# Kernel optimization log

Measured on AMD Instinct MI355X. Metric: run time of the kernel, lower is better.

## Reference

```python
import jax, jax.numpy as jnp
import numpy as np


def setup_inputs() -> dict:
    key = jax.random.key(0)
    k1, k2, k3, k4, k5 = jax.random.split(key, 5)
    return {
        "d1": jax.random.normal(k1, (2, 4096, 512), dtype=jnp.float32),
        "d2": jax.random.normal(k2, (2, 512, 4096), dtype=jnp.float32),
        "d3": jax.random.normal(k3, (2, 4096, 512), dtype=jnp.float32),
        "d4": jax.random.normal(k4, (512, 512), dtype=jnp.float32),
        "d5": jax.random.normal(k5, (1, 512), dtype=jnp.float32),
    }


def reference(d1, d2, d3, d4, d5):
    # attention core: scores = d1 @ d2 -> [2, 4096, 4096]
    scores = jnp.einsum('bsd,bdt->bst', d1, d2)
    attn = jax.nn.softmax(scores, axis=2)
    # weighted values: [2, 4096, 512]
    ctx = jnp.einsum('bst,btd->bsd', attn, d3)
    # flatten batch*seq and apply final projection with bias (addmm)
    x = ctx.reshape(8192, 512)
    return d5 + x @ d4  # d5 [1,512] broadcasts over rows
```

## Files before the change

kernel.cpp:

```cpp
#include <hip/hip_runtime.h>

typedef unsigned short u16;
typedef __attribute__((ext_vector_type(8))) short short8;
typedef __attribute__((ext_vector_type(4))) float f32x4;

#define MFMA16(a, b, c) __builtin_amdgcn_mfma_f32_16x16x32_bf16((a), (b), (c), 0, 0, 0)

constexpr int Bb = 2, Ss = 4096, Tt = 4096, Dd = 512;
constexpr int BM = 64, BN = 64, TP = 4;
constexpr int TPART = Tt / TP;
constexpr int TCH = TPART / BN;

constexpr size_t SZ_BF = (size_t)Bb * Ss * Dd * 2;
constexpr size_t O_QH  = 0;
constexpr size_t O_QL  = O_QH + SZ_BF;
constexpr size_t O_D2TH = O_QL + SZ_BF;
constexpr size_t O_D2TL = O_D2TH + SZ_BF;
constexpr size_t O_D3T  = O_D2TL + SZ_BF;
constexpr size_t O_D4T  = O_D3T + SZ_BF;
constexpr size_t O_CTX  = O_D4T + (size_t)512 * 512 * 2;
constexpr size_t O_OP   = O_CTX + SZ_BF;
constexpr size_t O_MP   = O_OP + (size_t)TP * SZ_BF;
constexpr size_t O_LP   = O_MP + (size_t)TP * Bb * Ss * 4;

__device__ __forceinline__ u16 f2bf(float x) {
  union { float f; unsigned u; } v; v.f = x;
  unsigned r = v.u + 0x7fffu + ((v.u >> 16) & 1u);
  return (u16)(r >> 16);
}
__device__ __forceinline__ float bf2f(u16 h) {
  union { unsigned u; float f; } v; v.u = ((unsigned)h) << 16;
  return v.f;
}

__global__ void cvt_split_kernel(const float* __restrict__ in,
                                 u16* __restrict__ outh, u16* __restrict__ outl) {
  const int i = blockIdx.x * 256 + threadIdx.x;
  float4 v = ((const float4*)in)[i];
  ushort4 hh, ll;
  hh.x = f2bf(v.x); ll.x = f2bf(v.x - bf2f(hh.x));
  hh.y = f2bf(v.y); ll.y = f2bf(v.y - bf2f(hh.y));
  hh.z = f2bf(v.z); ll.z = f2bf(v.z - bf2f(hh.z));
  hh.w = f2bf(v.w); ll.w = f2bf(v.w - bf2f(hh.w));
  ((ushort4*)outh)[i] = hh;
  ((ushort4*)outl)[i] = ll;
}

__global__ void transpose_split_kernel(const float* __restrict__ in,
                                       u16* __restrict__ outh,
                                       u16* __restrict__ outl,
                                       int R, int C) {
  __shared__ float tile[32][33];
  int b = blockIdx.z;
  const float* inb = in + (size_t)b * R * C;
  int x = blockIdx.x * 32 + threadIdx.x;
  int y0 = blockIdx.y * 32;
  for (int j = threadIdx.y; j < 32; j += 8)
    tile[j][threadIdx.x] = inb[(size_t)(y0 + j) * C + x];
  __syncthreads();
  size_t ob = (size_t)b * C * R;
  for (int j = threadIdx.y; j < 32; j += 8) {
    float v = tile[threadIdx.x][j];
    size_t oi = ob + (size_t)(blockIdx.x * 32 + j) * R + (y0 + threadIdx.x);
    u16 h = f2bf(v);
    outh[oi] = h;
    if (outl) outl[oi] = f2bf(v - bf2f(h));
  }
}

__global__ __launch_bounds__(256, 2)
void flash_part_kernel(const u16* __restrict__ qh_g,
                       const u16* __restrict__ ql_g,
                       const u16* __restrict__ d2th,
                       const u16* __restrict__ d2tl,
                       const u16* __restrict__ d3t,
                       u16* __restrict__ opart,
                       float* __restrict__ mpart,
                       float* __restrict__ lpart) {
  __shared__ u16 kh[64 * 136], kl[64 * 136];
  __shared__ u16 vb[128 * 72];
  __shared__ u16 ph[64 * 72];

  const int tid = threadIdx.x;
  const int wave = tid >> 6, lane = tid & 63, quad = lane >> 4, l15 = lane & 15;
  const int m0 = wave * 16;
  const int s0 = blockIdx.x * BM, tp = blockIdx.y, b = blockIdx.z;

  f32x4 o_acc[32];
#pragma unroll
  for (int i = 0; i < 32; i++) o_acc[i] = (f32x4){0.f, 0.f, 0.f, 0.f};
  float m_r[4] = {-INFINITY, -INFINITY, -INFINITY, -INFINITY};
  float l_r[4] = {0.f, 0.f, 0.f, 0.f};

  const u16* qh_row = qh_g + ((size_t)b * Ss + s0 + m0 + l15) * Dd + quad * 8;
  const u16* ql_row = ql_g + ((size_t)b * Ss + s0 + m0 + l15) * Dd + quad * 8;
  const u16* kh_b = d2th + (size_t)b * Tt * Dd;
  const u16* kl_b = d2tl + (size_t)b * Tt * Dd;
  const u16* v_b  = d3t  + (size_t)b * Dd * Tt;

  const int krow = tid >> 2, kcol = (tid & 3) * 32;
  const int vrow = tid >> 1, vcol = (tid & 1) * 32;

  for (int tc = 0; tc < TCH; tc++) {
    const int t0 = tp * TPART + tc * BN;
    f32x4 s_acc[4];
#pragma unroll
    for (int nt = 0; nt < 4; nt++) s_acc[nt] = (f32x4){0.f, 0.f, 0.f, 0.f};

    for (int ds = 0; ds < 4; ds++) {
      const int d0 = ds * 128;
      __syncthreads();
      {
        const u16* sh = kh_b + (size_t)(t0 + krow) * Dd + d0 + kcol;
        const u16* sl = kl_b + (size_t)(t0 + krow) * Dd + d0 + kcol;
        u16* dh = &kh[krow * 136 + kcol];
        u16* dl = &kl[krow * 136 + kcol];
#pragma unroll
        for (int u = 0; u < 32; u += 8) {
          *(uint4*)(dh + u) = *(const uint4*)(sh + u);
          *(uint4*)(dl + u) = *(const uint4*)(sl + u);
        }
      }
      __syncthreads();
      short8 ah[4], al[4];
#pragma unroll
      for (int ks = 0; ks < 4; ks++) {
        ah[ks] = *(const short8*)(qh_row + d0 + ks * 32);
        al[ks] = *(const short8*)(ql_row + d0 + ks * 32);
      }
#pragma unroll
      for (int ks = 0; ks < 4; ks++) {
        const int kk = ks * 32 + quad * 8;
#pragma unroll
        for (int nt = 0; nt < 4; nt++) {
          short8 bh = *(const short8*)&kh[(nt * 16 + l15) * 136 + kk];
          short8 bl = *(const short8*)&kl[(nt * 16 + l15) * 136 + kk];
          s_acc[nt] = MFMA16(ah[ks], bh, s_acc[nt]);
          s_acc[nt] = MFMA16(al[ks], bh, s_acc[nt]);
          s_acc[nt] = MFMA16(ah[ks], bl, s_acc[nt]);
        }
      }
    }

    float alpha[4], psum[4];
#pragma unroll
    for (int r = 0; r < 4; r++) {
      float v = fmaxf(fmaxf(s_acc[0][r], s_acc[1][r]), fmaxf(s_acc[2][r], s_acc[3][r]));
      v = fmaxf(v, __shfl_xor(v, 1));
      v = fmaxf(v, __shfl_xor(v, 2));
      v = fmaxf(v, __shfl_xor(v, 4));
      v = fmaxf(v, __shfl_xor(v, 8));
      float mn = fmaxf(m_r[r], v);
      alpha[r] = __expf(m_r[r] - mn);
      m_r[r] = mn;
      psum[r] = 0.f;
    }
#pragma unroll
    for (int nt = 0; nt < 4; nt++) {
#pragma unroll
      for (int r = 0; r < 4; r++) {
        float p = __expf(s_acc[nt][r] - m_r[r]);
        psum[r] += p;
        ph[(m0 + quad * 4 + r) * 72 + nt * 16 + l15] = f2bf(p);
      }
    }
#pragma unroll
    for (int r = 0; r < 4; r++) {
      float v = psum[r];
      v += __shfl_xor(v, 1);
      v += __shfl_xor(v, 2);
      v += __shfl_xor(v, 4);
      v += __shfl_xor(v, 8);
      l_r[r] = l_r[r] * alpha[r] + v;
    }
#pragma unroll
    for (int j = 0; j < 32; j++) {
#pragma unroll
      for (int r = 0; r < 4; r++) o_acc[j][r] *= alpha[r];
    }

#pragma unroll
    for (int nc = 0; nc < 4; nc++) {
      __syncthreads();
      {
        const u16* sv = v_b + (size_t)(nc * 128 + vrow) * Tt + t0 + vcol;
        u16* dv = &vb[vrow * 72 + vcol];
#pragma unroll
        for (int u = 0; u < 32; u += 8) *(uint4*)(dv + u) = *(const uint4*)(sv + u);
      }
      __syncthreads();
#pragma unroll
      for (int ks = 0; ks < 2; ks++) {
        const int kk = ks * 32 + quad * 8;
        short8 ap = *(const short8*)&ph[(m0 + l15) * 72 + kk];
#pragma unroll
        for (int nt = 0; nt < 8; nt++) {
          short8 bv = *(const short8*)&vb[(nt * 16 + l15) * 72 + kk];
          o_acc[nc * 8 + nt] = MFMA16(ap, bv, o_acc[nc * 8 + nt]);
        }
      }
    }
  }

  const size_t obase = (((size_t)tp * Bb + b) * Ss + s0) * Dd;
#pragma unroll
  for (int j = 0; j < 32; j++) {
    const int col = (j >> 3) * 128 + (j & 7) * 16 + l15;
#pragma unroll
    for (int r = 0; r < 4; r++) {
      const int row = m0 + quad * 4 + r;
      opart[obase + (size_t)row * Dd + col] = f2bf(o_acc[j][r]);
    }
  }
  if (l15 == 0) {
    const size_t sbase = ((size_t)tp * Bb + b) * Ss + s0;
#pragma unroll
    for (int r = 0; r < 4; r++) {
      const int row = m0 + quad * 4 + r;
      mpart[sbase + row] = m_r[r];
      lpart[sbase + row] = l_r[r];
    }
  }
}

__global__ void combine_kernel(const u16* __restrict__ opart,
                               const float* __restrict__ mpart,
                               const float* __restrict__ lpart,
                               u16* __restrict__ ctx) {
  const int idx = blockIdx.x * blockDim.x + threadIdx.x;
  const int vpr = Dd / 8;
  const int row = idx / vpr;
  const int dv = (idx % vpr) * 8;
  float mv[TP], mM = -INFINITY;
#pragma unroll
  for (int p = 0; p < TP; p++) {
    mv[p] = mpart[(size_t)p * Bb * Ss + row];
    mM = fmaxf(mM, mv[p]);
  }
  float w[TP], denom = 0.f;
#pragma unroll
  for (int p = 0; p < TP; p++) {
    float e = __expf(mv[p] - mM);
    w[p] = e;
    denom += e * lpart[(size_t)p * Bb * Ss + row];
  }
  const float inv = 1.0f / denom;
  float acc[8];
#pragma unroll
  for (int e = 0; e < 8; e++) acc[e] = 0.f;
#pragma unroll
  for (int p = 0; p < TP; p++) {
    uint4 raw = *(const uint4*)&opart[(size_t)p * Bb * Ss * Dd + (size_t)row * Dd + dv];
    const u16* u = (const u16*)&raw;
#pragma unroll
    for (int e = 0; e < 8; e++) acc[e] += w[p] * bf2f(u[e]);
  }
  u16 outv[8];
#pragma unroll
  for (int e = 0; e < 8; e++) outv[e] = f2bf(acc[e] * inv);
  *(uint4*)&ctx[(size_t)row * Dd + dv] = *(const uint4*)outv;
}

__global__ __launch_bounds__(256, 2)
void proj_kernel(const u16* __restrict__ ctx,
                 const u16* __restrict__ d4t,
                 const float* __restrict__ d5,
                 float* __restrict__ out) {
  __shared__ u16 a_lds[128 * 40], b_lds[128 * 40];
  const int tid = threadIdx.x;
  const int wave = tid >> 6, lane = tid & 63, quad = lane >> 4, l15 = lane & 15;
  const int m0w = (wave & 1) * 64, n0w = (wave >> 1) * 64;
  const int bm = blockIdx.x, bn = blockIdx.y;
  f32x4 acc[4][4];
#pragma unroll
  for (int i = 0; i < 4; i++)
#pragma unroll
    for (int j = 0; j < 4; j++) acc[i][j] = (f32x4){0.f, 0.f, 0.f, 0.f};

  const int srow = tid >> 2, scol = (tid & 3) * 8;
  for (int kt = 0; kt < 16; kt++) {
    const int k0 = kt * 32;
    __syncthreads();
#pragma unroll
    for (int pass = 0; pass < 2; pass++) {
      const int row = srow + pass * 64;
      *(uint4*)&a_lds[row * 40 + scol] =
          *(const uint4*)&ctx[(size_t)(bm * 128 + row) * Dd + k0 + scol];
      *(uint4*)&b_lds[row * 40 + scol] =
          *(const uint4*)&d4t[(size_t)(bn * 128 + row) * Dd + k0 + scol];
    }
    __syncthreads();
    short8 af[4], bfr[4];
#pragma unroll
    for (int i = 0; i < 4; i++)
      af[i] = *(const short8*)&a_lds[(m0w + 16 * i + l15) * 40 + quad * 8];
#pragma unroll
    for (int j = 0; j < 4; j++)
      bfr[j] = *(const short8*)&b_lds[(n0w + 16 * j + l15) * 40 + quad * 8];
#pragma unroll
    for (int i = 0; i < 4; i++)
#pragma unroll
      for (int j = 0; j < 4; j++) acc[i][j] = MFMA16(af[i], bfr[j], acc[i][j]);
  }
#pragma unroll
  for (int j = 0; j < 4; j++) {
    const int colg = bn * 128 + n0w + 16 * j + l15;
    const float bias = d5[colg];
#pragma unroll
    for (int i = 0; i < 4; i++) {
#pragma unroll
      for (int r = 0; r < 4; r++) {
        const int rowg = bm * 128 + m0w + 16 * i + quad * 4 + r;
        out[(size_t)rowg * 512 + colg] = acc[i][j][r] + bias;
      }
    }
  }
}

extern "C" void kernel_launch(void* const* d_in, const int* in_sizes, int n_in,
                              void* d_out, int out_size, void* d_ws, size_t ws_size,
                              hipStream_t stream) {
  (void)in_sizes; (void)n_in; (void)out_size; (void)ws_size;
  const float* d1 = (const float*)d_in[0];
  const float* d2 = (const float*)d_in[1];
  const float* d3 = (const float*)d_in[2];
  const float* d4 = (const float*)d_in[3];
  const float* d5 = (const float*)d_in[4];
  float* out = (float*)d_out;
  char* ws = (char*)d_ws;

  u16* qh_g = (u16*)(ws + O_QH);
  u16* ql_g = (u16*)(ws + O_QL);
  u16* d2th = (u16*)(ws + O_D2TH);
  u16* d2tl = (u16*)(ws + O_D2TL);
  u16* d3t  = (u16*)(ws + O_D3T);
  u16* d4t  = (u16*)(ws + O_D4T);
  u16* ctx  = (u16*)(ws + O_CTX);
  u16* opart = (u16*)(ws + O_OP);
  float* mpart = (float*)(ws + O_MP);
  float* lpart = (float*)(ws + O_LP);

  cvt_split_kernel<<<(Bb * Ss * Dd / 4) / 256, 256, 0, stream>>>(d1, qh_g, ql_g);
  transpose_split_kernel<<<dim3(128, 16, 2), dim3(32, 8), 0, stream>>>(d2, d2th, d2tl, 512, 4096);
  transpose_split_kernel<<<dim3(16, 128, 2), dim3(32, 8), 0, stream>>>(d3, d3t, nullptr, 4096, 512);
  transpose_split_kernel<<<dim3(16, 16, 1), dim3(32, 8), 0, stream>>>(d4, d4t, nullptr, 512, 512);

  flash_part_kernel<<<dim3(Ss / BM, TP, Bb), 256, 0, stream>>>(qh_g, ql_g, d2th, d2tl, d3t,
                                                               opart, mpart, lpart);
  combine_kernel<<<(Bb * Ss * Dd / 8) / 256, 256, 0, stream>>>(opart, mpart, lpart, ctx);
  proj_kernel<<<dim3(64, 4), 256, 0, stream>>>(ctx, d4t, d5, out);
}
```

Baseline: 516.9 us.

## Swizzle LDS tiles for K, V and P, and raise wave priority around MFMA

Writes the K-high/K-low, V and probability tiles into LDS with a rotating 8-element group swizzle on top of the existing padding, and applies the same index mapping on the MFMA operand reads. The goal is fewer LDS bank conflicts on the short8 fragment loads. The P fragments are now loaded once per key chunk rather than once per value chunk, and the Q register loads move ahead of the barrier. s_setprio brackets the MFMA loops so waves issuing matrix instructions get scheduling priority. This adds some integer index arithmetic per load.

Measured after the change: 560.9 us. 1.09x slower.

```diff
diff --git a/kernel.cpp b/kernel.cpp
--- a/kernel.cpp
+++ b/kernel.cpp
@@ -113,33 +113,38 @@
       {
         const u16* sh = kh_b + (size_t)(t0 + krow) * Dd + d0 + kcol;
         const u16* sl = kl_b + (size_t)(t0 + krow) * Dd + d0 + kcol;
-        u16* dh = &kh[krow * 136 + kcol];
-        u16* dl = &kl[krow * 136 + kcol];
-#pragma unroll
-        for (int u = 0; u < 32; u += 8) {
-          *(uint4*)(dh + u) = *(const uint4*)(sh + u);
-          *(uint4*)(dl + u) = *(const uint4*)(sl + u);
+        const int gb = kcol >> 3;
+#pragma unroll
+        for (int j = 0; j < 4; j++) {
+          const int g = gb + j;
+          const int s = ((g + 2 * krow) & 7) | (g & 8);
+          *(uint4*)&kh[krow * 136 + s * 8] = *(const uint4*)(sh + j * 8);
+          *(uint4*)&kl[krow * 136 + s * 8] = *(const uint4*)(sl + j * 8);
         }
       }
-      __syncthreads();
       short8 ah[4], al[4];
 #pragma unroll
       for (int ks = 0; ks < 4; ks++) {
         ah[ks] = *(const short8*)(qh_row + d0 + ks * 32);
         al[ks] = *(const short8*)(ql_row + d0 + ks * 32);
       }
+      __syncthreads();
+      __builtin_amdgcn_s_setprio(1);
 #pragma unroll
       for (int ks = 0; ks < 4; ks++) {
-        const int kk = ks * 32 + quad * 8;
+        const int g0 = ks * 4 + quad;
+        const int sg = ((g0 + 2 * l15) & 7) | (g0 & 8);
 #pragma unroll
         for (int nt = 0; nt < 4; nt++) {
-          short8 bh = *(const short8*)&kh[(nt * 16 + l15) * 136 + kk];
-          short8 bl = *(const short8*)&kl[(nt * 16 + l15) * 136 + kk];
+          const int off = (nt * 16 + l15) * 136 + sg * 8;
+          short8 bh = *(const short8*)&kh[off];
+          short8 bl = *(const short8*)&kl[off];
           s_acc[nt] = MFMA16(ah[ks], bh, s_acc[nt]);
           s_acc[nt] = MFMA16(al[ks], bh, s_acc[nt]);
           s_acc[nt] = MFMA16(ah[ks], bl, s_acc[nt]);
         }
       }
+      __builtin_amdgcn_s_setprio(0);
     }
 
     float alpha[4], psum[4];
@@ -161,7 +166,8 @@
       for (int r = 0; r < 4; r++) {
         float p = __expf(s_acc[nt][r] - m_r[r]);
         psum[r] += p;
-        ph[(m0 + quad * 4 + r) * 72 + nt * 16 + l15] = f2bf(p);
+        const int sp = (2 * nt + (l15 >> 3) + 2 * r) & 7;
+        ph[(m0 + quad * 4 + r) * 72 + sp * 8 + (l15 & 7)] = f2bf(p);
       }
     }
 #pragma unroll
@@ -179,26 +185,40 @@
       for (int r = 0; r < 4; r++) o_acc[j][r] *= alpha[r];
     }
 
+    short8 ap[2];
+#pragma unroll
+    for (int ks = 0; ks < 2; ks++) {
+      const int g0 = ks * 4 + quad;
+      const int sg = (g0 + 2 * l15) & 7;
+      ap[ks] = *(const short8*)&ph[(m0 + l15) * 72 + sg * 8];
+    }
+
 #pragma unroll
     for (int nc = 0; nc < 4; nc++) {
       __syncthreads();
       {
         const u16* sv = v_b + (size_t)(nc * 128 + vrow) * Tt + t0 + vcol;
-        u16* dv = &vb[vrow * 72 + vcol];
-#pragma unroll
-        for (int u = 0; u < 32; u += 8) *(uint4*)(dv + u) = *(const uint4*)(sv + u);
+        const int gb = vcol >> 3;
+#pragma unroll
+        for (int j = 0; j < 4; j++) {
+          const int g = gb + j;
+          const int s = (g + 2 * vrow) & 7;
+          *(uint4*)&vb[vrow * 72 + s * 8] = *(const uint4*)(sv + j * 8);
+        }
       }
       __syncthreads();
+      __builtin_amdgcn_s_setprio(1);
 #pragma unroll
       for (int ks = 0; ks < 2; ks++) {
-        const int kk = ks * 32 + quad * 8;
-        short8 ap = *(const short8*)&ph[(m0 + l15) * 72 + kk];
+        const int g0 = ks * 4 + quad;
+        const int sg = (g0 + 2 * l15) & 7;
 #pragma unroll
         for (int nt = 0; nt < 8; nt++) {
-          short8 bv = *(const short8*)&vb[(nt * 16 + l15) * 72 + kk];
-          o_acc[nc * 8 + nt] = MFMA16(ap, bv, o_acc[nc * 8 + nt]);
+          short8 bv = *(const short8*)&vb[(nt * 16 + l15) * 72 + sg * 8];
+          o_acc[nc * 8 + nt] = MFMA16(ap[ks], bv, o_acc[nc * 8 + nt]);
         }
       }
+      __builtin_amdgcn_s_setprio(0);
     }
   }
 
```

## Double-buffer K/V tiles with async global-to-LDS loads and XOR swizzle

Applied to the files above, without the earlier changes.

Replaces the synchronous register-staged K and V tile loads with direct global-to-LDS loads into a two-slot ring buffer. The next K slice or V chunk is issued before the current one is consumed, so memory latency can overlap the MFMA work, and one barrier per stage is removed. The LDS padding is replaced by an XOR swizzle for the K, V and P tiles to avoid bank conflicts without extra space. The cost is a more complex buffer schedule whose correctness depends on the barriers also waiting for the outstanding async loads.

Measured after the change: 672.4 us. 30.1% more time.

```diff
diff --git a/kernel.cpp b/kernel.cpp
--- a/kernel.cpp
+++ b/kernel.cpp
@@ -31,6 +31,11 @@
 __device__ __forceinline__ float bf2f(u16 h) {
   union { unsigned u; float f; } v; v.u = ((unsigned)h) << 16;
   return v.f;
+}
+
+__device__ __forceinline__ void gl_lds16(const u16* g, u16* l) {
+  __builtin_amdgcn_global_load_lds((const __attribute__((address_space(1))) void*)g,
+                                   (__attribute__((address_space(3))) void*)l, 16, 0, 0);
 }
 
 __global__ void cvt_split_kernel(const float* __restrict__ in,
@@ -77,14 +82,14 @@
                        u16* __restrict__ opart,
                        float* __restrict__ mpart,
                        float* __restrict__ lpart) {
-  __shared__ u16 kh[64 * 136], kl[64 * 136];
-  __shared__ u16 vb[128 * 72];
-  __shared__ u16 ph[64 * 72];
+  __shared__ __align__(1024) u16 ring[2][16384];
+  __shared__ __align__(16) u16 ph[64 * 64];
 
   const int tid = threadIdx.x;
   const int wave = tid >> 6, lane = tid & 63, quad = lane >> 4, l15 = lane & 15;
   const int m0 = wave * 16;
   const int s0 = blockIdx.x * BM, tp = blockIdx.y, b = blockIdx.z;
+  const int x7 = l15 & 7;
 
   f32x4 o_acc[32];
 #pragma unroll
@@ -98,48 +103,66 @@
   const u16* kl_b = d2tl + (size_t)b * Tt * Dd;
   const u16* v_b  = d3t  + (size_t)b * Dd * Tt;
 
-  const int krow = tid >> 2, kcol = (tid & 3) * 32;
-  const int vrow = tid >> 1, vcol = (tid & 1) * 32;
+  const int klr = lane >> 4, ks16 = lane & 15;
+  const int vlr = lane >> 3, vs8 = lane & 7;
+
+  auto issueK = [&](int t0_, int d0_, int p) {
+#pragma unroll
+    for (int i = 0; i < 4; i++) {
+      const int r = wave * 16 + i * 4 + klr;
+      const int gs = ((ks16 & 7) ^ (r & 7)) | (ks16 & 8);
+      const size_t so = (size_t)(t0_ + r) * Dd + d0_ + gs * 8;
+      gl_lds16(kh_b + so, &ring[p][(wave * 16 + i * 4) * 128]);
+      gl_lds16(kl_b + so, &ring[p][8192 + (wave * 16 + i * 4) * 128]);
+    }
+  };
+  auto issueV = [&](int t0_, int nc, int p, int h) {
+#pragma unroll
+    for (int i = 0; i < 4; i++) {
+      const int r = wave * 32 + i * 8 + vlr;
+      const int gs = vs8 ^ (r & 7);
+      gl_lds16(v_b + (size_t)(nc * 128 + r) * Tt + t0_ + gs * 8,
+               &ring[p][h * 8192 + (wave * 32 + i * 8) * 64]);
+    }
+  };
+
+  const int t00 = tp * TPART;
+  issueK(t00, 0, 0);
+  __syncthreads();
 
   for (int tc = 0; tc < TCH; tc++) {
-    const int t0 = tp * TPART + tc * BN;
+    const int t0 = t00 + tc * BN;
+    const int t0n = t00 + ((tc + 1 < TCH) ? tc + 1 : 0) * BN;
     f32x4 s_acc[4];
 #pragma unroll
     for (int nt = 0; nt < 4; nt++) s_acc[nt] = (f32x4){0.f, 0.f, 0.f, 0.f};
 
     for (int ds = 0; ds < 4; ds++) {
+      const int p = ds & 1;
       const int d0 = ds * 128;
-      __syncthreads();
-      {
-        const u16* sh = kh_b + (size_t)(t0 + krow) * Dd + d0 + kcol;
-        const u16* sl = kl_b + (size_t)(t0 + krow) * Dd + d0 + kcol;
-        u16* dh = &kh[krow * 136 + kcol];
-        u16* dl = &kl[krow * 136 + kcol];
-#pragma unroll
-        for (int u = 0; u < 32; u += 8) {
-          *(uint4*)(dh + u) = *(const uint4*)(sh + u);
-          *(uint4*)(dl + u) = *(const uint4*)(sl + u);
-        }
-      }
-      __syncthreads();
       short8 ah[4], al[4];
 #pragma unroll
       for (int ks = 0; ks < 4; ks++) {
         ah[ks] = *(const short8*)(qh_row + d0 + ks * 32);
         al[ks] = *(const short8*)(ql_row + d0 + ks * 32);
       }
-#pragma unroll
-      for (int ks = 0; ks < 4; ks++) {
-        const int kk = ks * 32 + quad * 8;
+      if (ds < 3) issueK(t0, d0 + 128, p ^ 1);
+      else        issueV(t0, 0, 0, 0);
+#pragma unroll
+      for (int a = 0; a < 4; a++) {
+        const int G = a * 4 + quad;
+        const int sg = ((G & 7) ^ x7) | (G & 8);
 #pragma unroll
         for (int nt = 0; nt < 4; nt++) {
-          short8 bh = *(const short8*)&kh[(nt * 16 + l15) * 136 + kk];
-          short8 bl = *(const short8*)&kl[(nt * 16 + l15) * 136 + kk];
-          s_acc[nt] = MFMA16(ah[ks], bh, s_acc[nt]);
-          s_acc[nt] = MFMA16(al[ks], bh, s_acc[nt]);
-          s_acc[nt] = MFMA16(ah[ks], bl, s_acc[nt]);
+          const int off = (nt * 16 + l15) * 128 + sg * 8;
+          short8 bh = *(const short8*)&ring[p][off];
+          short8 bl = *(const short8*)&ring[p][8192 + off];
+          s_acc[nt] = MFMA16(ah[a], bh, s_acc[nt]);
+          s_acc[nt] = MFMA16(al[a], bh, s_acc[nt]);
+          s_acc[nt] = MFMA16(ah[a], bl, s_acc[nt]);
         }
       }
+      __syncthreads();
     }
 
     float alpha[4], psum[4];
@@ -161,7 +184,9 @@
       for (int r = 0; r < 4; r++) {
         float p = __expf(s_acc[nt][r] - m_r[r]);
         psum[r] += p;
-        ph[(m0 + quad * 4 + r) * 72 + nt * 16 + l15] = f2bf(p);
+        const int row = m0 + quad * 4 + r;
+        const int c = nt * 16 + l15;
+        ph[row * 64 + (((c >> 3) ^ (row & 7)) << 3) + (c & 7)] = f2bf(p);
       }
     }
 #pragma unroll
@@ -181,24 +206,20 @@
 
 #pragma unroll
     for (int nc = 0; nc < 4; nc++) {
-      __syncthreads();
-      {
-        const u16* sv = v_b + (size_t)(nc * 128 + vrow) * Tt + t0 + vcol;
-        u16* dv = &vb[vrow * 72 + vcol];
-#pragma unroll
-        for (int u = 0; u < 32; u += 8) *(uint4*)(dv + u) = *(const uint4*)(sv + u);
-      }
-      __syncthreads();
+      const int p = nc >> 1, h = nc & 1;
+      if (nc < 3) issueV(t0, nc + 1, (nc + 1) >> 1, (nc + 1) & 1);
+      else        issueK(t0n, 0, 0);
 #pragma unroll
       for (int ks = 0; ks < 2; ks++) {
-        const int kk = ks * 32 + quad * 8;
-        short8 ap = *(const short8*)&ph[(m0 + l15) * 72 + kk];
+        const int sg = ((ks * 4 + quad) ^ x7) << 3;
+        short8 ap = *(const short8*)&ph[(m0 + l15) * 64 + sg];
 #pragma unroll
         for (int nt = 0; nt < 8; nt++) {
-          short8 bv = *(const short8*)&vb[(nt * 16 + l15) * 72 + kk];
+          short8 bv = *(const short8*)&ring[p][h * 8192 + (nt * 16 + l15) * 64 + sg];
           o_acc[nc * 8 + nt] = MFMA16(ap, bv, o_acc[nc * 8 + nt]);
         }
       }
+      __syncthreads();
     }
   }
 
```

## Double-buffer V tiles and prefetch next K chunk to overlap loads with MFMA

Applied to the files above, without the earlier changes.

Splits the V shared-memory tile into two buffers so the next V chunk is loaded into registers during the current P·V MFMAs, then stored to the alternate buffer. It also stages the first K chunk of the next tile during the last V step, which removes one barrier pair per stage. The goal is to hide global-load latency behind compute. In exchange it uses more LDS and registers, which may reduce occupancy at 2 blocks per CU. The barrier placement needs careful checking: the ph write and the K/V staging buffers are reused across phases.

Result: slower. 553.7 us (+7.1%).

```diff
diff --git a/kernel.cpp b/kernel.cpp
--- a/kernel.cpp
+++ b/kernel.cpp
@@ -78,7 +78,7 @@
                        float* __restrict__ mpart,
                        float* __restrict__ lpart) {
   __shared__ u16 kh[64 * 136], kl[64 * 136];
-  __shared__ u16 vb[128 * 72];
+  __shared__ u16 vbA[128 * 72], vbB[128 * 72];
   __shared__ u16 ph[64 * 72];
 
   const int tid = threadIdx.x;
@@ -101,33 +101,76 @@
   const int krow = tid >> 2, kcol = (tid & 3) * 32;
   const int vrow = tid >> 1, vcol = (tid & 1) * 32;
 
+  auto stageK = [&](int t0_, int d0_) {
+    const u16* sh = kh_b + (size_t)(t0_ + krow) * Dd + d0_ + kcol;
+    const u16* sl = kl_b + (size_t)(t0_ + krow) * Dd + d0_ + kcol;
+    u16* dh = &kh[krow * 136 + kcol];
+    u16* dl = &kl[krow * 136 + kcol];
+#pragma unroll
+    for (int u = 0; u < 32; u += 8) {
+      *(uint4*)(dh + u) = *(const uint4*)(sh + u);
+      *(uint4*)(dl + u) = *(const uint4*)(sl + u);
+    }
+  };
+  auto loadV = [&](int t0_, int nc, uint4* r) {
+    const u16* sv = v_b + (size_t)(nc * 128 + vrow) * Tt + t0_ + vcol;
+#pragma unroll
+    for (int j = 0; j < 4; j++) r[j] = *(const uint4*)(sv + j * 8);
+  };
+  auto storeV = [&](u16* vb, const uint4* r) {
+    u16* dv = &vb[vrow * 72 + vcol];
+#pragma unroll
+    for (int j = 0; j < 4; j++) *(uint4*)(dv + j * 8) = r[j];
+  };
+
+  const int t00 = tp * TPART;
+  stageK(t00, 0);
+
   for (int tc = 0; tc < TCH; tc++) {
-    const int t0 = tp * TPART + tc * BN;
+    const int t0 = t00 + tc * BN;
+    const int t0n = t00 + ((tc + 1 < TCH) ? tc + 1 : 0) * BN;
     f32x4 s_acc[4];
 #pragma unroll
     for (int nt = 0; nt < 4; nt++) s_acc[nt] = (f32x4){0.f, 0.f, 0.f, 0.f};
 
-    for (int ds = 0; ds < 4; ds++) {
+    {
+      short8 ah[4], al[4];
+#pragma unroll
+      for (int ks = 0; ks < 4; ks++) {
+        ah[ks] = *(const short8*)(qh_row + ks * 32);
+        al[ks] = *(const short8*)(ql_row + ks * 32);
+      }
+      __syncthreads();
+#pragma unroll
+      for (int ks = 0; ks < 4; ks++) {
+        const int kk = ks * 32 + quad * 8;
+#pragma unroll
+        for (int nt = 0; nt < 4; nt++) {
+          short8 bh = *(const short8*)&kh[(nt * 16 + l15) * 136 + kk];
+          short8 bl = *(const short8*)&kl[(nt * 16 + l15) * 136 + kk];
+          s_acc[nt] = MFMA16(ah[ks], bh, s_acc[nt]);
+          s_acc[nt] = MFMA16(al[ks], bh, s_acc[nt]);
+          s_acc[nt] = MFMA16(ah[ks], bl, s_acc[nt]);
+        }
+      }
+    }
+
+    for (int ds = 1; ds < 4; ds++) {
       const int d0 = ds * 128;
       __syncthreads();
-      {
-        const u16* sh = kh_b + (size_t)(t0 + krow) * Dd + d0 + kcol;
-        const u16* sl = kl_b + (size_t)(t0 + krow) * Dd + d0 + kcol;
-        u16* dh = &kh[krow * 136 + kcol];
-        u16* dl = &kl[krow * 136 + kcol];
-#pragma unroll
-        for (int u = 0; u < 32; u += 8) {
-          *(uint4*)(dh + u) = *(const uint4*)(sh + u);
-          *(uint4*)(dl + u) = *(const uint4*)(sl + u);
-        }
-      }
-      __syncthreads();
+      stageK(t0, d0);
+      if (ds == 3) {
+        uint4 vr[4];
+        loadV(t0, 0, vr);
+        storeV(vbA, vr);
+      }
       short8 ah[4], al[4];
 #pragma unroll
       for (int ks = 0; ks < 4; ks++) {
         ah[ks] = *(const short8*)(qh_row + d0 + ks * 32);
         al[ks] = *(const short8*)(ql_row + d0 + ks * 32);
       }
+      __syncthreads();
 #pragma unroll
       for (int ks = 0; ks < 4; ks++) {
         const int kk = ks * 32 + quad * 8;
@@ -182,23 +225,21 @@
 #pragma unroll
     for (int nc = 0; nc < 4; nc++) {
       __syncthreads();
-      {
-        const u16* sv = v_b + (size_t)(nc * 128 + vrow) * Tt + t0 + vcol;
-        u16* dv = &vb[vrow * 72 + vcol];
-#pragma unroll
-        for (int u = 0; u < 32; u += 8) *(uint4*)(dv + u) = *(const uint4*)(sv + u);
-      }
-      __syncthreads();
+      uint4 vr[4];
+      if (nc < 3) loadV(t0, nc + 1, vr);
+      else        stageK(t0n, 0);
+      const u16* vbR = (nc & 1) ? vbB : vbA;
 #pragma unroll
       for (int ks = 0; ks < 2; ks++) {
         const int kk = ks * 32 + quad * 8;
         short8 ap = *(const short8*)&ph[(m0 + l15) * 72 + kk];
 #pragma unroll
         for (int nt = 0; nt < 8; nt++) {
-          short8 bv = *(const short8*)&vb[(nt * 16 + l15) * 72 + kk];
+          short8 bv = *(const short8*)&vbR[(nt * 16 + l15) * 72 + kk];
           o_acc[nc * 8 + nt] = MFMA16(ap, bv, o_acc[nc * 8 + nt]);
         }
       }
+      if (nc < 3) storeV((nc & 1) ? vbA : vbB, vr);
     }
   }
 
```
